# Performance work log

Measured on AMD Instinct MI355X. Metric: run time of the kernel, lower is better.

## Reference

```python
import jax, jax.numpy as jnp
import numpy as np

STRIDE = 1
PADDING = 1
GROUPS = 1


def setup_inputs() -> dict:
    key = jax.random.key(0)
    kx, kw, kb = jax.random.split(key, 3)
    x_int = jax.random.randint(kx, (16, 256, 56, 56), 0, 127, dtype=jnp.int32)
    weight_int = jax.random.randint(kw, (256, 256, 3, 3), 0, 127, dtype=jnp.int32)
    bias_int = jax.random.randint(kb, (256,), 0, 127, dtype=jnp.int32)
    return {"x_int": x_int, "weight_int": weight_int, "bias_int": bias_int}


def reference(x_int, weight_int, bias_int):
    # Integer conv2d with int32 accumulation, exactly F.conv2d semantics.
    y = jax.lax.conv_general_dilated(
        x_int,
        weight_int,
        window_strides=(STRIDE, STRIDE),
        padding=((PADDING, PADDING), (PADDING, PADDING)),
        dimension_numbers=("NCHW", "OIHW", "NCHW"),
        feature_group_count=GROUPS,
    )
    # bias broadcast over [B, Cout, H, W]
    return y + bias_int[None, :, None, None]
```

## Files before the change

### kernel.cpp

```cpp
#include <hip/hip_runtime.h>


typedef int v4i  __attribute__((ext_vector_type(4)));
typedef int v16i __attribute__((ext_vector_type(16)));

#define X8_ROWSTRIDE 1856
#define X8_IMGSTRIDE 107648
#define X8_BYTES     13778944
#define W8_CHUNK     18432
#define W8_COTILE    147456
#define WBUF         36864
#define XBUF         20480
#define LBUF         57344

typedef const __attribute__((address_space(1))) unsigned char* gptr_t;
typedef __attribute__((address_space(3))) unsigned char* lptr_t;

__device__ __forceinline__ void gll(const unsigned char* g, unsigned char* l) {
  __builtin_amdgcn_global_load_lds((gptr_t)g, (lptr_t)l, 16, 0, 0);
}

__device__ __forceinline__ int pack4(const int* p, int stride) {
  return (p[0] & 255) | ((p[stride] & 255) << 8) |
         ((p[2 * stride] & 255) << 16) | ((p[3 * stride] & 255) << 24);
}

__global__ __launch_bounds__(256)
void pack_all(const int* __restrict__ x, const int* __restrict__ wgt,
              unsigned char* __restrict__ ws8) {
  const int blk = blockIdx.x;
  if (blk < 784) {
    const int gid = blk * 256 + threadIdx.x;
    const int srcg = gid & 1;
    int t = gid >> 1;
    const int sq = t % 14;  t /= 14;
    const int row = t % 56 + 1;
    const int cb  = t / 56;
    const int chunk = cb >> 4, b = cb & 15;
    const int ci0 = chunk * 32 + srcg * 16;
    const int* src = x + (b * 256 + ci0) * 3136 + (row - 1) * 56 + 4 * sq;
    v4i L[16];
    #pragma unroll
    for (int ch = 0; ch < 16; ++ch) L[ch] = *(const v4i*)(src + ch * 3136);
    unsigned char* dstrow = ws8 + cb * X8_IMGSTRIDE + row * X8_ROWSTRIDE;
    #pragma unroll
    for (int j = 0; j < 4; ++j) {
      const int slot = 4 * sq + 1 + j;
      v4i g;
      #pragma unroll
      for (int d = 0; d < 4; ++d)
        g[d] = (L[4 * d][j] & 255) | ((L[4 * d + 1][j] & 255) << 8) |
               ((L[4 * d + 2][j] & 255) << 16) | ((L[4 * d + 3][j] & 255) << 24);
      const int p = (srcg + (slot >> 2)) & 1;
      *(v4i*)(dstrow + slot * 32 + p * 16) = g;
    }
  } else if (blk < 1012) {
    const int g2 = (blk - 784) * 256 + threadIdx.x;
    const int cb = g2 / 456;
    const int r  = g2 - cb * 456;
    int off;
    if (r < 232) {
      const int row = r < 116 ? 0 : 57;
      const int rr = r % 116;
      off = row * X8_ROWSTRIDE + (rr >> 1) * 32 + (rr & 1) * 16;
    } else {
      const int r2 = r - 232;
      const int row = (r2 >> 2) + 1;
      const int slot = (r2 & 2) ? 57 : 0;
      off = row * X8_ROWSTRIDE + slot * 32 + (r2 & 1) * 16;
    }
    *(v4i*)(ws8 + cb * X8_IMGSTRIDE + off) = (v4i){0, 0, 0, 0};
  } else {
    const int gw = (blk - 1012) * 256 + threadIdx.x;
    const int p = gw & 1;
    int t = gw >> 1;
    const int tap = t % 9;  t /= 9;
    const int co = t & 63;
    const int tcc = t >> 6;
    const int chunk = tcc & 7, cotile = tcc >> 3;
    const int srcg = (p + (co >> 2)) & 1;
    const int ci0 = chunk * 32 + srcg * 16;
    const int* src = wgt + ((cotile * 64 + co) * 256 + ci0) * 9 + tap;
    v4i v = (v4i){pack4(src, 9), pack4(src + 36, 9),
                  pack4(src + 72, 9), pack4(src + 108, 9)};
    *(v4i*)(ws8 + X8_BYTES + (t * 9 + tap) * 32 + p * 16) = v;
  }
}

__device__ __forceinline__ void stage_chunk(const unsigned char* wa,
                                            const unsigned char* wb,
                                            const unsigned char* xg,
                                            unsigned char* ldsb, int c, int buf,
                                            int tid) {
  const unsigned char* wsa = wa + c * W8_CHUNK;
  const unsigned char* wsb = wb + c * W8_CHUNK;
  const unsigned char* xsrc = xg + c * (16 * X8_IMGSTRIDE);
  unsigned char* wdst = ldsb + buf * LBUF;
  unsigned char* xdst = wdst + WBUF;
  #pragma unroll
  for (int i = 0; i < 4; ++i) {
    const int o = (tid + i * 256) * 16;
    gll(wsa + o, wdst + o);
  }
  if (tid < 128) {
    const int o = (1024 + tid) * 16;
    gll(wsa + o, wdst + o);
  } else {
    const int o = (tid - 128) * 16;
    gll(wsb + o, wdst + W8_CHUNK + o);
  }
  #pragma unroll
  for (int i = 0; i < 4; ++i) {
    const int o = (128 + tid + i * 256) * 16;
    gll(wsb + o, wdst + W8_CHUNK + o);
  }
  #pragma unroll
  for (int i = 0; i < 5; ++i) {
    const int o = (tid + i * 256) * 16;
    gll(xsrc + o, xdst + o);
  }
}

__global__ __launch_bounds__(256, 1)
void conv_main(const unsigned char* __restrict__ ws8, const int* __restrict__ bias,
               int* __restrict__ out) {
  __shared__ __align__(16) unsigned char lds[2 * LBUF];
  __shared__ int bls[128];

  const int tid = threadIdx.x, lane = tid & 63, wv = tid >> 6;
  const int n = lane & 31, gq = lane >> 5;
  const int tc = blockIdx.y;
  const int hb = blockIdx.x;
  const int hg = hb >> 4, b = hb & 15;
  const int h0 = hg * 8;

  if (tid < 128) bls[tid] = bias[tc * 128 + tid];
  asm volatile("s_waitcnt lgkmcnt(0)" ::: "memory");

  const int abase = n * 288 + (((gq + (n >> 2)) & 1) << 4);
  int boff[3][4];
  #pragma unroll
  for (int kw = 0; kw < 3; ++kw)
    #pragma unroll
    for (int bt = 0; bt < 4; ++bt) {
      int slot = bt * 16 + (n & 15) + kw;
      if (slot > 57) slot = 57;
      boff[kw][bt] = slot * 32 + (((gq + (slot >> 2)) & 1) << 4);
    }
  const int rbase = (2 * wv + (n >> 4)) * X8_ROWSTRIDE;

  v16i acc[4][4];
  #pragma unroll
  for (int i = 0; i < 4; ++i)
    #pragma unroll
    for (int j = 0; j < 4; ++j)
      acc[i][j] = (v16i){0,0,0,0,0,0,0,0,0,0,0,0,0,0,0,0};

  const unsigned char* wa = ws8 + X8_BYTES + (2 * tc) * W8_COTILE;
  const unsigned char* wb = wa + W8_COTILE;
  const unsigned char* xg = ws8 + b * X8_IMGSTRIDE + h0 * X8_ROWSTRIDE;

  stage_chunk(wa, wb, xg, lds, 0, 0, tid);
  int buf = 0;
  #pragma unroll 1
  for (int c = 0; c < 8; ++c) {
    if (c < 7) {
      stage_chunk(wa, wb, xg, lds, c + 1, buf ^ 1, tid);
      asm volatile("s_waitcnt vmcnt(14)" ::: "memory");
    } else {
      asm volatile("s_waitcnt vmcnt(0)" ::: "memory");
    }
    __builtin_amdgcn_s_barrier();
    asm volatile("" ::: "memory");
    const unsigned char* wls = lds + buf * LBUF;
    const unsigned char* xs  = wls + WBUF;
    #pragma unroll
    for (int kh = 0; kh < 3; ++kh) {
      const unsigned char* xr = xs + rbase + kh * X8_ROWSTRIDE;
      #pragma unroll
      for (int kw = 0; kw < 3; ++kw) {
        const int tap = kh * 3 + kw;
        v4i a[4];
        #pragma unroll
        for (int q = 0; q < 4; ++q)
          a[q] = *(const v4i*)(wls + q * 9216 + abase + tap * 32);
        #pragma unroll
        for (int bt = 0; bt < 4; ++bt) {
          const v4i bb = *(const v4i*)(xr + boff[kw][bt]);
          #pragma unroll
          for (int q = 0; q < 4; ++q)
            acc[q][bt] = __builtin_amdgcn_mfma_i32_32x32x32_i8(a[q], bb, acc[q][bt], 0, 0, 0);
        }
      }
    }
    asm volatile("" ::: "memory");
    __builtin_amdgcn_s_barrier();
    buf ^= 1;
  }

  const int h = h0 + 2 * wv + (n >> 4);
  const int wbase = lane & 15;
  #pragma unroll
  for (int q = 0; q < 4; ++q) {
    #pragma unroll
    for (int r = 0; r < 16; ++r) {
      const int co = q * 32 + (r & 3) + 8 * (r >> 2) + 4 * gq;
      const int bv = bls[co];
      int* orow = out + ((b * 256 + tc * 128 + co) * 56 + h) * 56;
      #pragma unroll
      for (int bt = 0; bt < 4; ++bt) {
        const int w0 = bt * 16 + wbase;
        if (w0 < 56) orow[w0] = acc[q][bt][r] + bv;
      }
    }
  }
}

extern "C" void kernel_launch(void* const* d_in, const int* in_sizes, int n_in,
                              void* d_out, int out_size, void* d_ws, size_t ws_size,
                              hipStream_t stream) {
  const int* x    = (const int*)d_in[0];
  const int* w    = (const int*)d_in[1];
  const int* bias = (const int*)d_in[2];
  unsigned char* ws8 = (unsigned char*)d_ws;
  hipLaunchKernelGGL(pack_all, dim3(1156), dim3(256), 0, stream, x, w, ws8);
  hipLaunchKernelGGL(conv_main, dim3(112, 2, 1), dim3(256), 0, stream,
                     ws8, bias, (int*)d_out);
}
```

Before: 152.4 us.

## Use one barrier per chunk and double-buffer LDS fragments in registers

Each chunk iteration now starts with one vmcnt(0) wait and one barrier. The prefetch of the next chunk into the other LDS buffer is issued only after that barrier, so the trailing second barrier is no longer needed. Inside the chunk, the A and B fragments for the next tap are loaded into a second register set while the 16 MFMAs of the current tap run, with sched_group_barrier hints to interleave LDS reads and MFMAs. This aims to hide LDS read latency behind matrix work and cut synchronisation overhead. In exchange it uses about 64 more VGPRs and starts each prefetch slightly later in the iteration.

After: 144.1 us. 5.5% less time.

```diff
diff --git a/kernel.cpp b/kernel.cpp
--- a/kernel.cpp
+++ b/kernel.cpp
@@ -121,6 +121,20 @@
   }
 }
 
+#define LOADTAP(T, S)                                                     \
+  do {                                                                    \
+    const int kh_ = (T) / 3, kw_ = (T) % 3;                               \
+    const unsigned char* xr_ = xs + rbase + kh_ * X8_ROWSTRIDE;           \
+    fa[S][0] = *(const v4i*)(wls + 0 * 9216 + abase + (T) * 32);          \
+    fa[S][1] = *(const v4i*)(wls + 1 * 9216 + abase + (T) * 32);          \
+    fa[S][2] = *(const v4i*)(wls + 2 * 9216 + abase + (T) * 32);          \
+    fa[S][3] = *(const v4i*)(wls + 3 * 9216 + abase + (T) * 32);          \
+    fb[S][0] = *(const v4i*)(xr_ + boff[kw_][0]);                         \
+    fb[S][1] = *(const v4i*)(xr_ + boff[kw_][1]);                         \
+    fb[S][2] = *(const v4i*)(xr_ + boff[kw_][2]);                         \
+    fb[S][3] = *(const v4i*)(xr_ + boff[kw_][3]);                         \
+  } while (0)
+
 __global__ __launch_bounds__(256, 1)
 void conv_main(const unsigned char* __restrict__ ws8, const int* __restrict__ bias,
                int* __restrict__ out) {
@@ -164,37 +178,31 @@
   int buf = 0;
   #pragma unroll 1
   for (int c = 0; c < 8; ++c) {
-    if (c < 7) {
-      stage_chunk(wa, wb, xg, lds, c + 1, buf ^ 1, tid);
-      asm volatile("s_waitcnt vmcnt(14)" ::: "memory");
-    } else {
-      asm volatile("s_waitcnt vmcnt(0)" ::: "memory");
-    }
+    asm volatile("s_waitcnt vmcnt(0)" ::: "memory");
     __builtin_amdgcn_s_barrier();
     asm volatile("" ::: "memory");
-    const unsigned char* wls = lds + buf * LBUF;
-    const unsigned char* xs  = wls + WBUF;
-    #pragma unroll
-    for (int kh = 0; kh < 3; ++kh) {
-      const unsigned char* xr = xs + rbase + kh * X8_ROWSTRIDE;
+    if (c < 7) stage_chunk(wa, wb, xg, lds, c + 1, buf ^ 1, tid);
+    {
+      const unsigned char* wls = lds + buf * LBUF;
+      const unsigned char* xs  = wls + WBUF;
+      v4i fa[2][4], fb[2][4];
+      LOADTAP(0, 0);
+      __builtin_amdgcn_sched_group_barrier(0x100, 8, 0);
       #pragma unroll
-      for (int kw = 0; kw < 3; ++kw) {
-        const int tap = kh * 3 + kw;
-        v4i a[4];
+      for (int tap = 0; tap < 9; ++tap) {
+        const int cur = tap & 1, nxt = cur ^ 1;
+        if (tap < 8) {
+          LOADTAP(tap + 1, nxt);
+          __builtin_amdgcn_sched_group_barrier(0x100, 8, 0);
+        }
         #pragma unroll
         for (int q = 0; q < 4; ++q)
-          a[q] = *(const v4i*)(wls + q * 9216 + abase + tap * 32);
-        #pragma unroll
-        for (int bt = 0; bt < 4; ++bt) {
-          const v4i bb = *(const v4i*)(xr + boff[kw][bt]);
           #pragma unroll
-          for (int q = 0; q < 4; ++q)
-            acc[q][bt] = __builtin_amdgcn_mfma_i32_32x32x32_i8(a[q], bb, acc[q][bt], 0, 0, 0);
-        }
+          for (int bt = 0; bt < 4; ++bt)
+            acc[q][bt] = __builtin_amdgcn_mfma_i32_32x32x32_i8(fa[cur][q], fb[cur][bt], acc[q][bt], 0, 0, 0);
+        __builtin_amdgcn_sched_group_barrier(0x008, 16, 0);
       }
     }
-    asm volatile("" ::: "memory");
-    __builtin_amdgcn_s_barrier();
     buf ^= 1;
   }
 
```
